# Performance work log

Measured on AMD Instinct MI355X. Metric: run time of the kernel, lower is better.

## Reference

```python
import jax, jax.numpy as jnp
import numpy as np

B, T, D = 4, 2048, 2048
NH, NKV, HD = 8, 4, 256
SOFT_CAP = 50.0
ROPE_BASE = 10000
K_MASK = -2.3819763e38


def apply_rope(x, positions, base_frequency):
    # x: [b, t, n, h], positions: [b, t]
    head_dim = x.shape[-1]
    fraction = 2.0 * jnp.arange(head_dim // 2, dtype=jnp.float32) / head_dim
    timescale = base_frequency ** fraction  # [h/2]
    sinusoid = positions[..., None].astype(jnp.float32) / timescale  # [b, t, h/2]
    sinusoid = sinusoid[..., None, :]  # [b, t, 1, h/2]
    sin, cos = jnp.sin(sinusoid), jnp.cos(sinusoid)
    x1, x2 = jnp.split(x, 2, axis=-1)
    out = jnp.concatenate([x1 * cos - x2 * sin, x2 * cos + x1 * sin], axis=-1)
    return out.astype(x.dtype)


def setup_inputs() -> dict:
    key = jax.random.key(0)
    k1, k2, k3 = jax.random.split(key, 3)
    x = jax.random.normal(k1, (B, T, D), dtype=jnp.float32)
    positions = jnp.broadcast_to(jnp.arange(T, dtype=jnp.int32), (B, T))
    # causal mask, broadcast over kv-head axis
    causal = jnp.tril(jnp.ones((T, T), dtype=bool))
    attn_mask = jnp.broadcast_to(causal[None, None], (B, 1, T, T))
    w_qkv = jax.random.normal(k2, (D, (NH + 2 * NKV) * HD), dtype=jnp.float32) * (D ** -0.5)
    w_out = jax.random.normal(k3, (NH * HD, D), dtype=jnp.float32) * ((NH * HD) ** -0.5)
    return {"x": x, "positions": positions, "attn_mask": attn_mask,
            "w_qkv": w_qkv, "w_out": w_out}


def reference(x, positions, attn_mask, w_qkv, w_out):
    b, t, _ = x.shape
    g = NH // NKV  # queries per kv head
    qkv = x @ w_qkv  # [b, t, (NH+2*NKV)*HD]
    q, k, v = jnp.split(qkv, [NH * HD, (NH + NKV) * HD], axis=-1)
    q = q.reshape(b, t, NH, HD)
    k = k.reshape(b, t, NKV, HD)
    v = v.reshape(b, t, NKV, HD)
    q = apply_rope(q, positions, ROPE_BASE)
    k = apply_rope(k, positions, ROPE_BASE)
    q_grouped = q.reshape(b, t, NKV, g, HD)
    logits = jnp.einsum('btkgh,bskh->bkgts', q_grouped, k,
                        preferred_element_type=jnp.float32)
    # soft-cap BEFORE scaling (faithful to source order)
    logits = jnp.tanh(logits / SOFT_CAP) * SOFT_CAP
    logits = logits / jnp.sqrt(jnp.float32(HD))
    final_mask = attn_mask[:, :, None, :, :]  # [b, 1, 1, t, s]
    masked = jnp.where(final_mask, logits, K_MASK)
    probs = jax.nn.softmax(masked, axis=-1).astype(x.dtype)
    encoded = jnp.einsum('bkgts,bskh->btkgh', probs, v)
    encoded = encoded.reshape(b, t, NH * HD)
    return encoded @ w_out
```

## Files before the change

kernel.cpp:

```cpp
#include <hip/hip_runtime.h>
#include <hip/hip_bf16.h>

typedef unsigned short u16;
typedef unsigned int   u32;
typedef __bf16 bf16x8 __attribute__((ext_vector_type(8)));
typedef float  f32x4  __attribute__((ext_vector_type(4)));

static constexpr int B_ = 4, T_ = 2048, D_ = 2048, NH_ = 8, NKV_ = 4, HD_ = 256;
static constexpr int QKVC = (NH_ + 2 * NKV_) * HD_;
static constexpr int ENC_C = NH_ * HD_;

__device__ __forceinline__ u16 f2b(float f) {
  u32 x = __float_as_uint(f);
  return (u16)((x + 0x7fffu + ((x >> 16) & 1u)) >> 16);
}
__device__ __forceinline__ float b2f(u16 u) { return __uint_as_float(((u32)u) << 16); }

__device__ __forceinline__ void gload_lds16(const void* g, void* l) {
  __builtin_amdgcn_global_load_lds((const __attribute__((address_space(1))) void*)g,
                                   (__attribute__((address_space(3))) void*)l, 16, 0, 0);
}

__global__ void cvt_f32_bf16(const float* __restrict__ in, u16* __restrict__ out, int n) {
  for (size_t i = ((size_t)blockIdx.x * 256 + threadIdx.x) * 8; i < (size_t)n;
       i += (size_t)gridDim.x * 256 * 8) {
    float4 a = *(const float4*)(in + i);
    float4 b = *(const float4*)(in + i + 4);
    u16 t[8] = {f2b(a.x), f2b(a.y), f2b(a.z), f2b(a.w), f2b(b.x), f2b(b.y), f2b(b.z), f2b(b.w)};
    *(uint4*)(out + i) = *(const uint4*)t;
  }
}

__global__ void transpose_cvt(const float* __restrict__ src, u16* __restrict__ dst, int R, int C) {
  __shared__ u16 tl[64][72];
  const int c0 = blockIdx.x << 6, r0 = blockIdx.y << 6;
  const int tid = threadIdx.x;
  const int lr = tid >> 2, lc = (tid & 3) << 4;
  const float* p = src + (size_t)(r0 + lr) * C + c0 + lc;
#pragma unroll
  for (int j = 0; j < 16; j += 4) {
    float4 v = *(const float4*)(p + j);
    tl[lr][lc + j + 0] = f2b(v.x);
    tl[lr][lc + j + 1] = f2b(v.y);
    tl[lr][lc + j + 2] = f2b(v.z);
    tl[lr][lc + j + 3] = f2b(v.w);
  }
  __syncthreads();
  u16 tmp[16];
#pragma unroll
  for (int j = 0; j < 16; j++) tmp[j] = tl[lc + j][lr];
  u16* q = dst + (size_t)(c0 + lr) * R + r0 + lc;
  *(uint4*)q = *(const uint4*)tmp;
  *(uint4*)(q + 8) = *(const uint4*)(tmp + 8);
}

__global__ void vt_build(const u16* __restrict__ qkv, u16* __restrict__ vt) {
  __shared__ u16 tl[64][72];
  const int t0 = blockIdx.x << 6, d0 = blockIdx.y << 6, z = blockIdx.z;
  const int tid = threadIdx.x;
  const int lr = tid >> 2, lc = (tid & 3) << 4;
  const u16* p = qkv + (size_t)((z >> 2) * T_ + t0 + lr) * QKVC + (NH_ + NKV_) * HD_ +
                 (z & 3) * HD_ + d0 + lc;
#pragma unroll
  for (int j = 0; j < 16; j++) tl[lr][lc + j] = p[j];
  __syncthreads();
  u16 tmp[16];
#pragma unroll
  for (int j = 0; j < 16; j++) tmp[j] = tl[lc + j][lr];
  u16* q = vt + ((size_t)z * HD_ + d0 + lr) * T_ + t0 + lc;
  *(uint4*)q = *(const uint4*)tmp;
  *(uint4*)(q + 8) = *(const uint4*)(tmp + 8);
}

__global__ void rope_inplace(u16* __restrict__ qkv, const int* __restrict__ positions) {
  const int row = blockIdx.x;
  const float pos = (float)positions[row];
  u16* base = qkv + (size_t)row * QKVC;
  for (int it = threadIdx.x; it < 12 * 128; it += 256) {
    const int head = it >> 7, i = it & 127;
    const int cb = head * HD_;
    const float inv = exp2f(-(float)i * 0.10381025296522975f);
    const float ang = pos * inv;
    float s, c;
    __sincosf(ang, &s, &c);
    const float x1 = b2f(base[cb + i]), x2 = b2f(base[cb + 128 + i]);
    base[cb + i]       = f2b(x1 * c - x2 * s);
    base[cb + 128 + i] = f2b(x2 * c + x1 * s);
  }
}

template <bool OUT_F32>
__global__ __launch_bounds__(256, 2) void gemm_bt(const u16* __restrict__ A,
                                                  const u16* __restrict__ Bt,
                                                  void* __restrict__ Cp, int M, int N, int K) {
  __shared__ __align__(16) u16 Al[2][128 * 32];
  __shared__ __align__(16) u16 Bl[2][128 * 32];
  const int tid = threadIdx.x;
  const int w = tid >> 6, l = tid & 63;
  const int lr = l & 15, khi = l >> 4;
  const size_t bm = (size_t)blockIdx.y << 7, bn = (size_t)blockIdx.x << 7;
  const int mrow = (w >> 1) << 6, ncol = (w & 1) << 6;
  f32x4 acc[4][4] = {};
  const int nt = K >> 5;

  auto stage = [&](int buf, int k0) {
#pragma unroll
    for (int j = 0; j < 2; j++) {
      const int p = j * 256 + tid;
      const int row = p >> 2, slot = p & 3;
      const int dk = slot ^ ((row >> 1) & 3);
      gload_lds16(A + (bm + row) * K + k0 + dk * 8, &Al[buf][(j * 256 + (w << 6)) * 8]);
      gload_lds16(Bt + (bn + row) * K + k0 + dk * 8, &Bl[buf][(j * 256 + (w << 6)) * 8]);
    }
  };

  stage(0, 0);
  for (int t = 0; t < nt; ++t) {
    const int cur = t & 1;
    __syncthreads();
    if (t + 1 < nt) stage(cur ^ 1, (t + 1) << 5);
    bf16x8 aF[4], bF[4];
#pragma unroll
    for (int mf = 0; mf < 4; mf++) {
      const int r = mrow + (mf << 4) + lr;
      const int slot = khi ^ ((r >> 1) & 3);
      aF[mf] = *(const bf16x8*)&Al[cur][r * 32 + slot * 8];
    }
#pragma unroll
    for (int nf = 0; nf < 4; nf++) {
      const int c = ncol + (nf << 4) + lr;
      const int slot = khi ^ ((c >> 1) & 3);
      bF[nf] = *(const bf16x8*)&Bl[cur][c * 32 + slot * 8];
    }
#pragma unroll
    for (int mf = 0; mf < 4; mf++)
#pragma unroll
      for (int nf = 0; nf < 4; nf++)
        acc[mf][nf] = __builtin_amdgcn_mfma_f32_16x16x32_bf16(aF[mf], bF[nf], acc[mf][nf], 0, 0, 0);
  }
#pragma unroll
  for (int mf = 0; mf < 4; mf++) {
#pragma unroll
    for (int j = 0; j < 4; j++) {
      const size_t row = bm + mrow + (mf << 4) + (khi << 2) + j;
#pragma unroll
      for (int nf = 0; nf < 4; nf++) {
        const size_t col = bn + ncol + (nf << 4) + lr;
        if constexpr (OUT_F32)
          ((float*)Cp)[row * N + col] = acc[mf][nf][j];
        else
          ((u16*)Cp)[row * N + col] = f2b(acc[mf][nf][j]);
      }
    }
  }
}

__global__ __launch_bounds__(512, 2) void attn_kernel(const u16* __restrict__ qkv,
                                                      const u16* __restrict__ VT,
                                                      u16* __restrict__ enc) {
  __shared__ __align__(16) u16 Kl[2][16384];
  __shared__ __align__(16) u16 Vl[2][16384];
  const int tid = threadIdx.x, w = tid >> 6, l = tid & 63;
  const int lr = l & 15, khi = l >> 4;
  const int id = blockIdx.x;
  const int xcd = id & 7, slot = id >> 3;
  const int group = xcd + ((slot >> 4) << 3), sub = slot & 15;
  const int b = group >> 2, kv = group & 3;
  const int h = (kv << 1) + (sub & 1), qb = sub >> 1;
  const int chunk = (w < 4) ? qb : (15 - qb);
  const int qw = (chunk << 7) + ((w & 3) << 5);
  const int qmax = qw + 31;
  const int nst = 32 - 2 * qb;

  bf16x8 qf[2][8];
#pragma unroll
  for (int qg = 0; qg < 2; qg++) {
    const u16* qrow = qkv + (size_t)(b * T_ + qw + qg * 16 + lr) * QKVC + h * HD_ + khi * 8;
#pragma unroll
    for (int kk = 0; kk < 8; kk++) qf[qg][kk] = *(const bf16x8*)(qrow + kk * 32);
  }

  int offK[4], offV[4];
#pragma unroll
  for (int j = 0; j < 4; j++) {
    const int gg = j * 8 + w;
    const int sg = gg >> 3, kk = gg & 7;
    const int srow = ((sg >> 1) << 5) + ((sg & 1) << 2) + ((lr >> 2) << 3) + (lr & 3);
    offK[j] = srow * QKVC + kk * 32 + khi * 8;
    const int ks = gg >> 4, nf = gg & 15;
    offV[j] = ((nf << 4) + lr) * T_ + (ks << 5) + khi * 8;
  }
  const u16* Kp = qkv + (size_t)b * T_ * QKVC + NH_ * HD_ + kv * HD_;
  const u16* Vp = VT + (size_t)(b * NKV_ + kv) * HD_ * T_;

  f32x4 opv[2][16] = {};
  float lsum[2] = {0.f, 0.f};

  auto stage = [&](int bf, int st) {
    const u16* kp = Kp + (size_t)(st << 6) * QKVC;
    const u16* vp = Vp + (st << 6);
#pragma unroll
    for (int j = 0; j < 4; j++) {
      gload_lds16(kp + offK[j], &Kl[bf][(j * 8 + w) * 512]);
      gload_lds16(vp + offV[j], &Vl[bf][(j * 8 + w) * 512]);
    }
  };

  stage(0, 0);
  __syncthreads();
  int buf = 0;
  for (int st = 0; st < nst; ++st) {
    if (st + 1 < nst) stage(buf ^ 1, st + 1);
    const int s0 = st << 6;
    if (s0 <= qmax) {
      const u16* Kb = Kl[buf];
      const u16* Vb = Vl[buf];
#pragma unroll
      for (int ks = 0; ks < 2; ks++) {
        f32x4 pst[2][2] = {};
#pragma unroll
        for (int sgh = 0; sgh < 2; sgh++) {
          const int gb = ((ks << 1) + sgh) * 8;
#pragma unroll
          for (int kk = 0; kk < 8; kk++) {
            bf16x8 kf = *(const bf16x8*)&Kb[(gb + kk) * 512 + l * 8];
            pst[0][sgh] = __builtin_amdgcn_mfma_f32_16x16x32_bf16(kf, qf[0][kk], pst[0][sgh], 0, 0, 0);
            pst[1][sgh] = __builtin_amdgcn_mfma_f32_16x16x32_bf16(kf, qf[1][kk], pst[1][sgh], 0, 0, 0);
          }
        }
        union { u32 u[4]; bf16x8 v; } ap[2];
#pragma unroll
        for (int qg = 0; qg < 2; qg++) {
          const int tq = qw + qg * 16 + lr;
#pragma unroll
          for (int sgh = 0; sgh < 2; sgh++) {
#pragma unroll
            for (int j = 0; j < 4; j++) {
              const int s = s0 + ks * 32 + khi * 8 + sgh * 4 + j;
              const float e2 = __expf(pst[qg][sgh][j] * 0.04f);
              float p = __expf(-6.25f * __builtin_amdgcn_rcpf(e2 + 1.f));
              p = (s <= tq) ? p : 0.f;
              pst[qg][sgh][j] = p;
              lsum[qg] += p;
            }
          }
          ap[qg].u[0] = __builtin_amdgcn_perm(__float_as_uint(pst[qg][0][1]),
                                              __float_as_uint(pst[qg][0][0]), 0x07060302u);
          ap[qg].u[1] = __builtin_amdgcn_perm(__float_as_uint(pst[qg][0][3]),
                                              __float_as_uint(pst[qg][0][2]), 0x07060302u);
          ap[qg].u[2] = __builtin_amdgcn_perm(__float_as_uint(pst[qg][1][1]),
                                              __float_as_uint(pst[qg][1][0]), 0x07060302u);
          ap[qg].u[3] = __builtin_amdgcn_perm(__float_as_uint(pst[qg][1][3]),
                                              __float_as_uint(pst[qg][1][2]), 0x07060302u);
        }
#pragma unroll
        for (int nf = 0; nf < 16; nf++) {
          bf16x8 bv = *(const bf16x8*)&Vb[((ks << 4) + nf) * 512 + l * 8];
          opv[0][nf] = __builtin_amdgcn_mfma_f32_16x16x32_bf16(ap[0].v, bv, opv[0][nf], 0, 0, 0);
          opv[1][nf] = __builtin_amdgcn_mfma_f32_16x16x32_bf16(ap[1].v, bv, opv[1][nf], 0, 0, 0);
        }
      }
    }
    __syncthreads();
    buf ^= 1;
  }

#pragma unroll
  for (int qg = 0; qg < 2; qg++) {
    float s = lsum[qg];
    s += __shfl_xor(s, 16);
    s += __shfl_xor(s, 32);
    const float rinv = 1.f / s;
#pragma unroll
    for (int j = 0; j < 4; j++) {
      const float rj = __shfl(rinv, (khi << 2) + j);
      const size_t row = (size_t)(b * T_ + qw + qg * 16 + (khi << 2) + j) * ENC_C + h * HD_ + lr;
#pragma unroll
      for (int nf = 0; nf < 16; nf++) enc[row + (nf << 4)] = f2b(opv[qg][nf][j] * rj);
    }
  }
}

extern "C" void kernel_launch(void* const* d_in, const int* in_sizes, int n_in,
                              void* d_out, int out_size, void* d_ws, size_t ws_size,
                              hipStream_t stream) {
  const float* x = (const float*)d_in[0];
  const int* positions = (const int*)d_in[1];
  const float* w_qkv = (const float*)d_in[3];
  const float* w_out = (const float*)d_in[4];
  float* out = (float*)d_out;

  char* ws = (char*)d_ws;
  u16* X16 = (u16*)(ws + 0);
  u16* WQT = (u16*)(ws + 33554432);
  u16* WOT = (u16*)(ws + 50331648);
  u16* QKV = (u16*)(ws + 58720256);
  u16* VT  = (u16*)(ws + 125829120);
  u16* ENC = X16;

  cvt_f32_bf16<<<2048, 256, 0, stream>>>(x, X16, B_ * T_ * D_);
  {
    dim3 g(QKVC / 64, D_ / 64);
    transpose_cvt<<<g, 256, 0, stream>>>(w_qkv, WQT, D_, QKVC);
  }
  {
    dim3 g(D_ / 64, ENC_C / 64);
    transpose_cvt<<<g, 256, 0, stream>>>(w_out, WOT, ENC_C, D_);
  }
  {
    dim3 g(QKVC / 128, (B_ * T_) / 128);
    gemm_bt<false><<<g, 256, 0, stream>>>(X16, WQT, QKV, B_ * T_, QKVC, D_);
  }
  rope_inplace<<<B_ * T_, 256, 0, stream>>>(QKV, positions);
  {
    dim3 g(T_ / 64, HD_ / 64, B_ * NKV_);
    vt_build<<<g, 256, 0, stream>>>(QKV, VT);
  }
  attn_kernel<<<256, 512, 0, stream>>>(QKV, VT, ENC);
  {
    dim3 g(D_ / 128, (B_ * T_) / 128);
    gemm_bt<true><<<g, 256, 0, stream>>>(ENC, WOT, out, B_ * T_, D_, ENC_C);
  }
}
```

Before: 605.5 us.

## Replace GEMMs with 256x256 eight-wave pipelined kernel, vectorize RoPE, add setprio

Both projection GEMMs move to a new 512-thread kernel with 256x256 tiles, a 4-deep LDS ring with two tiles prefetched ahead, explicit vmcnt waits plus a raw s_barrier, XCD-aware block remapping, and s_setprio around the MFMA bursts. RoPE is rewritten so each thread handles 8 contiguous elements with 16-byte loads and stores. The attention kernel gains setprio hints around its MFMA loops. The larger tiles raise operand reuse and the deeper prefetch hides load latency. The price is higher register and LDS use, and the LDS swizzle is gone, which risks bank conflicts.

```diff
diff --git a/kernel.cpp b/kernel.cpp
--- a/kernel.cpp
+++ b/kernel.cpp
@@ -74,78 +74,120 @@
 
 __global__ void rope_inplace(u16* __restrict__ qkv, const int* __restrict__ positions) {
   const int row = blockIdx.x;
+  const int t = threadIdx.x;
+  if (t >= 192) return;
   const float pos = (float)positions[row];
-  u16* base = qkv + (size_t)row * QKVC;
-  for (int it = threadIdx.x; it < 12 * 128; it += 256) {
-    const int head = it >> 7, i = it & 127;
-    const int cb = head * HD_;
+  const int head = t >> 4, i8 = (t & 15) << 3;
+  u16* p1 = qkv + (size_t)row * QKVC + head * HD_ + i8;
+  u16* p2 = p1 + 128;
+  uint4 a = *(const uint4*)p1, b = *(const uint4*)p2;
+  u16 o1[8], o2[8];
+#pragma unroll
+  for (int j = 0; j < 8; j++) {
+    const int i = i8 + j;
     const float inv = exp2f(-(float)i * 0.10381025296522975f);
-    const float ang = pos * inv;
     float s, c;
-    __sincosf(ang, &s, &c);
-    const float x1 = b2f(base[cb + i]), x2 = b2f(base[cb + 128 + i]);
-    base[cb + i]       = f2b(x1 * c - x2 * s);
-    base[cb + 128 + i] = f2b(x2 * c + x1 * s);
-  }
+    __sincosf(pos * inv, &s, &c);
+    const float x1 = b2f(((const u16*)&a)[j]), x2 = b2f(((const u16*)&b)[j]);
+    o1[j] = f2b(x1 * c - x2 * s);
+    o2[j] = f2b(x2 * c + x1 * s);
+  }
+  *(uint4*)p1 = *(const uint4*)o1;
+  *(uint4*)p2 = *(const uint4*)o2;
 }
 
 template <bool OUT_F32>
-__global__ __launch_bounds__(256, 2) void gemm_bt(const u16* __restrict__ A,
-                                                  const u16* __restrict__ Bt,
-                                                  void* __restrict__ Cp, int M, int N, int K) {
-  __shared__ __align__(16) u16 Al[2][128 * 32];
-  __shared__ __align__(16) u16 Bl[2][128 * 32];
-  const int tid = threadIdx.x;
-  const int w = tid >> 6, l = tid & 63;
+__global__ __launch_bounds__(512, 2) void gemm8p(const u16* __restrict__ A,
+                                                 const u16* __restrict__ Bt,
+                                                 void* __restrict__ Cp, int M, int N, int K) {
+  __shared__ __align__(16) u16 Al[4][8192];
+  __shared__ __align__(16) u16 Bl[4][8192];
+  const int tid = threadIdx.x, wid = tid >> 6, l = tid & 63;
+  const int wm = wid >> 2, wn = wid & 3;
   const int lr = l & 15, khi = l >> 4;
-  const size_t bm = (size_t)blockIdx.y << 7, bn = (size_t)blockIdx.x << 7;
-  const int mrow = (w >> 1) << 6, ncol = (w & 1) << 6;
-  f32x4 acc[4][4] = {};
+
+  const int nwg = gridDim.x;
+  const int wg = (blockIdx.x & 7) * (nwg >> 3) + (blockIdx.x >> 3);
+  const int nbx = N >> 8;
+  const size_t bm = (size_t)(wg / nbx) << 8, bn = (size_t)(wg % nbx) << 8;
+
   const int nt = K >> 5;
-
-  auto stage = [&](int buf, int k0) {
-#pragma unroll
-    for (int j = 0; j < 2; j++) {
-      const int p = j * 256 + tid;
-      const int row = p >> 2, slot = p & 3;
-      const int dk = slot ^ ((row >> 1) & 3);
-      gload_lds16(A + (bm + row) * K + k0 + dk * 8, &Al[buf][(j * 256 + (w << 6)) * 8]);
-      gload_lds16(Bt + (bn + row) * K + k0 + dk * 8, &Bl[buf][(j * 256 + (w << 6)) * 8]);
-    }
+  f32x4 acc[8][4] = {};
+
+  const int srow = tid >> 2, scol = (tid & 3) << 3;
+  auto stage = [&](int buf, int kt) {
+    const size_t k0 = (size_t)kt << 5;
+    gload_lds16(A + (bm + srow) * K + k0 + scol, &Al[buf][tid * 8]);
+    gload_lds16(A + (bm + 128 + srow) * K + k0 + scol, &Al[buf][4096 + tid * 8]);
+    gload_lds16(Bt + (bn + srow) * K + k0 + scol, &Bl[buf][tid * 8]);
+    gload_lds16(Bt + (bn + 128 + srow) * K + k0 + scol, &Bl[buf][4096 + tid * 8]);
   };
 
   stage(0, 0);
+  stage(1, 1);
+
   for (int t = 0; t < nt; ++t) {
-    const int cur = t & 1;
-    __syncthreads();
-    if (t + 1 < nt) stage(cur ^ 1, (t + 1) << 5);
-    bf16x8 aF[4], bF[4];
-#pragma unroll
-    for (int mf = 0; mf < 4; mf++) {
-      const int r = mrow + (mf << 4) + lr;
-      const int slot = khi ^ ((r >> 1) & 3);
-      aF[mf] = *(const bf16x8*)&Al[cur][r * 32 + slot * 8];
-    }
-#pragma unroll
-    for (int nf = 0; nf < 4; nf++) {
-      const int c = ncol + (nf << 4) + lr;
-      const int slot = khi ^ ((c >> 1) & 3);
-      bF[nf] = *(const bf16x8*)&Bl[cur][c * 32 + slot * 8];
-    }
+    const int buf = t & 3;
+    if (t < nt - 1) {
+      asm volatile("s_waitcnt vmcnt(4)" ::: "memory");
+    } else {
+      asm volatile("s_waitcnt vmcnt(0)" ::: "memory");
+    }
+    __builtin_amdgcn_sched_barrier(0);
+    __builtin_amdgcn_s_barrier();
+    __builtin_amdgcn_sched_barrier(0);
+
+    const u16* Ab = Al[buf];
+    const u16* Bb = Bl[buf];
+    const bool pf = (t + 2 < nt);
+
+    if (pf) {
+      const size_t k0 = (size_t)(t + 2) << 5;
+      const int nb = (t + 2) & 3;
+      gload_lds16(A + (bm + srow) * K + k0 + scol, &Al[nb][tid * 8]);
+      gload_lds16(A + (bm + 128 + srow) * K + k0 + scol, &Al[nb][4096 + tid * 8]);
+    }
+    bf16x8 bF[4], aF[4];
+#pragma unroll
+    for (int nf = 0; nf < 4; nf++)
+      bF[nf] = *(const bf16x8*)&Bb[((wn << 6) + (nf << 4) + lr) * 32 + (khi << 3)];
+#pragma unroll
+    for (int mf = 0; mf < 4; mf++)
+      aF[mf] = *(const bf16x8*)&Ab[((wm << 7) + (mf << 4) + lr) * 32 + (khi << 3)];
+    __builtin_amdgcn_s_setprio(1);
 #pragma unroll
     for (int mf = 0; mf < 4; mf++)
 #pragma unroll
       for (int nf = 0; nf < 4; nf++)
         acc[mf][nf] = __builtin_amdgcn_mfma_f32_16x16x32_bf16(aF[mf], bF[nf], acc[mf][nf], 0, 0, 0);
-  }
-#pragma unroll
-  for (int mf = 0; mf < 4; mf++) {
+    __builtin_amdgcn_s_setprio(0);
+
+    if (pf) {
+      const size_t k0 = (size_t)(t + 2) << 5;
+      const int nb = (t + 2) & 3;
+      gload_lds16(Bt + (bn + srow) * K + k0 + scol, &Bl[nb][tid * 8]);
+      gload_lds16(Bt + (bn + 128 + srow) * K + k0 + scol, &Bl[nb][4096 + tid * 8]);
+    }
+#pragma unroll
+    for (int mf = 0; mf < 4; mf++)
+      aF[mf] = *(const bf16x8*)&Ab[((wm << 7) + ((mf + 4) << 4) + lr) * 32 + (khi << 3)];
+    __builtin_amdgcn_s_setprio(1);
+#pragma unroll
+    for (int mf = 0; mf < 4; mf++)
+#pragma unroll
+      for (int nf = 0; nf < 4; nf++)
+        acc[mf + 4][nf] = __builtin_amdgcn_mfma_f32_16x16x32_bf16(aF[mf], bF[nf], acc[mf + 4][nf], 0, 0, 0);
+    __builtin_amdgcn_s_setprio(0);
+  }
+
+#pragma unroll
+  for (int mf = 0; mf < 8; mf++) {
 #pragma unroll
     for (int j = 0; j < 4; j++) {
-      const size_t row = bm + mrow + (mf << 4) + (khi << 2) + j;
+      const size_t row = bm + (wm << 7) + (mf << 4) + (khi << 2) + j;
 #pragma unroll
       for (int nf = 0; nf < 4; nf++) {
-        const size_t col = bn + ncol + (nf << 4) + lr;
+        const size_t col = bn + (wn << 6) + (nf << 4) + lr;
         if constexpr (OUT_F32)
           ((float*)Cp)[row * N + col] = acc[mf][nf][j];
         else
@@ -218,6 +260,7 @@
 #pragma unroll
       for (int ks = 0; ks < 2; ks++) {
         f32x4 pst[2][2] = {};
+        __builtin_amdgcn_s_setprio(1);
 #pragma unroll
         for (int sgh = 0; sgh < 2; sgh++) {
           const int gb = ((ks << 1) + sgh) * 8;
@@ -228,6 +271,7 @@
             pst[1][sgh] = __builtin_amdgcn_mfma_f32_16x16x32_bf16(kf, qf[1][kk], pst[1][sgh], 0, 0, 0);
           }
         }
+        __builtin_amdgcn_s_setprio(0);
         union { u32 u[4]; bf16x8 v; } ap[2];
 #pragma unroll
         for (int qg = 0; qg < 2; qg++) {
@@ -253,12 +297,14 @@
           ap[qg].u[3] = __builtin_amdgcn_perm(__float_as_uint(pst[qg][1][3]),
                                               __float_as_uint(pst[qg][1][2]), 0x07060302u);
         }
+        __builtin_amdgcn_s_setprio(1);
 #pragma unroll
         for (int nf = 0; nf < 16; nf++) {
           bf16x8 bv = *(const bf16x8*)&Vb[((ks << 4) + nf) * 512 + l * 8];
           opv[0][nf] = __builtin_amdgcn_mfma_f32_16x16x32_bf16(ap[0].v, bv, opv[0][nf], 0, 0, 0);
           opv[1][nf] = __builtin_amdgcn_mfma_f32_16x16x32_bf16(ap[1].v, bv, opv[1][nf], 0, 0, 0);
         }
+        __builtin_amdgcn_s_setprio(0);
       }
     }
     __syncthreads();
@@ -307,18 +353,14 @@
     dim3 g(D_ / 64, ENC_C / 64);
     transpose_cvt<<<g, 256, 0, stream>>>(w_out, WOT, ENC_C, D_);
   }
-  {
-    dim3 g(QKVC / 128, (B_ * T_) / 128);
-    gemm_bt<false><<<g, 256, 0, stream>>>(X16, WQT, QKV, B_ * T_, QKVC, D_);
-  }
+  gemm8p<false><<<(B_ * T_ / 256) * (QKVC / 256), 512, 0, stream>>>(X16, WQT, QKV,
+                                                                    B_ * T_, QKVC, D_);
   rope_inplace<<<B_ * T_, 256, 0, stream>>>(QKV, positions);
   {
     dim3 g(T_ / 64, HD_ / 64, B_ * NKV_);
     vt_build<<<g, 256, 0, stream>>>(QKV, VT);
   }
   attn_kernel<<<256, 512, 0, stream>>>(QKV, VT, ENC);
-  {
-    dim3 g(D_ / 128, (B_ * T_) / 128);
-    gemm_bt<true><<<g, 256, 0, stream>>>(ENC, WOT, out, B_ * T_, D_, ENC_C);
-  }
-}
+  gemm8p<true><<<(B_ * T_ / 256) * (D_ / 256), 512, 0, stream>>>(ENC, WOT, out,
+                                                                 B_ * T_, D_, ENC_C);
+}
```

Measured after the change: 727.7 us. 1.2x slower.
